# Kernel optimization log

Measured on AMD Instinct MI355X. Metric: run time of the kernel, lower is better.

Reference implementation:

```python
import jax, jax.numpy as jnp
import numpy as np

EMB_DIM = 1024
N_HEADS = 16
N_KV_GROUPS = 4
GROUP_SIZE = N_HEADS // N_KV_GROUPS
HEAD_DIM = EMB_DIM // N_HEADS
KV_DIM = N_KV_GROUPS * HEAD_DIM
B, S = 2, 2048


def setup_inputs() -> dict:
    key = jax.random.key(0)
    ks = jax.random.split(key, 6)
    sc = 0.02
    return {
        "x": jax.random.normal(ks[0], (B, S, EMB_DIM), dtype=jnp.float32),
        "Wq": jax.random.normal(ks[1], (EMB_DIM, EMB_DIM), dtype=jnp.float32) * sc,
        "Wk": jax.random.normal(ks[2], (EMB_DIM, KV_DIM), dtype=jnp.float32) * sc,
        "Wv": jax.random.normal(ks[3], (EMB_DIM, KV_DIM), dtype=jnp.float32) * sc,
        "Wo": jax.random.normal(ks[4], (EMB_DIM, EMB_DIM), dtype=jnp.float32) * sc,
        "bo": jax.random.normal(ks[5], (EMB_DIM,), dtype=jnp.float32) * sc,
    }


def reference(x, Wq, Wk, Wv, Wo, bo):
    b, s, _ = x.shape
    # projections
    q = (x @ Wq).reshape(b, s, N_HEADS, HEAD_DIM).transpose(0, 2, 1, 3)      # [b,H,s,d]
    k = (x @ Wk).reshape(b, s, N_KV_GROUPS, HEAD_DIM).transpose(0, 2, 1, 3)  # [b,G,s,d]
    v = (x @ Wv).reshape(b, s, N_KV_GROUPS, HEAD_DIM).transpose(0, 2, 1, 3)
    # repeat_interleave KV heads to match query heads
    k = jnp.repeat(k, GROUP_SIZE, axis=1)  # [b,H,s,d]
    v = jnp.repeat(v, GROUP_SIZE, axis=1)
    scores = jnp.einsum("bhqd,bhkd->bhqk", q, k)  # [b,H,s,s]
    causal = jnp.triu(jnp.ones((s, s), dtype=bool), k=1)
    scores = jnp.where(causal, -jnp.inf, scores)
    attn = jax.nn.softmax(scores / np.sqrt(HEAD_DIM).astype(np.float32), axis=-1)
    ctx = jnp.einsum("bhqk,bhkd->bhqd", attn, v)  # [b,H,s,d]
    ctx = ctx.transpose(0, 2, 1, 3).reshape(b, s, EMB_DIM)
    return ctx @ Wo + bo
```

## Files before the change

### kernel.cpp

```cpp
#include <hip/hip_runtime.h>
#include <hip/hip_bf16.h>


typedef __attribute__((ext_vector_type(8))) short          bf16x8;
typedef __attribute__((ext_vector_type(4))) float          f32x4;
typedef __attribute__((ext_vector_type(4))) unsigned short u16x4;
typedef __attribute__((ext_vector_type(8))) unsigned short u16x8;

#define DEV __device__ __forceinline__

static constexpr int BB   = 2;
static constexpr int SS   = 2048;
static constexpr int EMB  = 1024;
static constexpr int QKVD = 1536;
static constexpr float SC2 = 0.18033688011112042f;
static constexpr float M2C = 16.0f;

DEV unsigned short f2b(float f) {
  union { float f; unsigned u; } v; v.f = f;
  unsigned r = (v.u + 0x7FFFu + ((v.u >> 16) & 1u)) >> 16;
  return (unsigned short)r;
}

DEV unsigned packbf2(float a, float b) {
  __hip_bfloat162 h = __float22bfloat162_rn(make_float2(a, b));
  union { __hip_bfloat162 h; unsigned u; } c; c.h = h; return c.u;
}

DEV void gl_lds16(const void* g, void* l) {
  __builtin_amdgcn_global_load_lds((__attribute__((address_space(1))) void*)g,
                                   (__attribute__((address_space(3))) void*)l,
                                   16, 0, 0);
}

__global__ __launch_bounds__(256) void prep_kernel(const float* __restrict__ x,
                                                   unsigned short* __restrict__ xb,
                                                   const float* __restrict__ Wq,
                                                   const float* __restrict__ Wk,
                                                   const float* __restrict__ Wv,
                                                   const float* __restrict__ Wo,
                                                   unsigned short* __restrict__ Wqkv_t,
                                                   unsigned short* __restrict__ Wo_t) {
  __shared__ unsigned short tile[64][72];
  const int blk = blockIdx.x;
  const int tid = threadIdx.x;
  if (blk < 2048) {
    size_t i = ((size_t)blk * 256 + tid) * 8;
    f32x4 f0 = *(const f32x4*)(x + i);
    f32x4 f1 = *(const f32x4*)(x + i + 4);
    u16x8 o;
    o[0] = f2b(f0[0]); o[1] = f2b(f0[1]); o[2] = f2b(f0[2]); o[3] = f2b(f0[3]);
    o[4] = f2b(f1[0]); o[5] = f2b(f1[1]); o[6] = f2b(f1[2]); o[7] = f2b(f1[3]);
    *(u16x8*)(xb + i) = o;
    return;
  }
  int idx = blk - 2048;
  const float* W; unsigned short* Dst; int N, kb, nb;
  if (idx < 256)      { W = Wq; Dst = Wqkv_t;                       N = 1024; kb = idx >> 4; nb = idx & 15; }
  else if (idx < 320) { int j = idx - 256; W = Wk; Dst = Wqkv_t + (size_t)1024 * 1024; N = 256; kb = j >> 2; nb = j & 3; }
  else if (idx < 384) { int j = idx - 320; W = Wv; Dst = Wqkv_t + (size_t)1280 * 1024; N = 256; kb = j >> 2; nb = j & 3; }
  else                { int j = idx - 384; W = Wo; Dst = Wo_t;      N = 1024; kb = j >> 4; nb = j & 15; }
  const int kb64 = kb * 64, nb64 = nb * 64;
#pragma unroll
  for (int p = 0; p < 16; ++p) {
    int i = tid + 256 * p;
    int k = i >> 6, n = i & 63;
    tile[k][n] = f2b(W[(size_t)(kb64 + k) * N + nb64 + n]);
  }
  __syncthreads();
#pragma unroll
  for (int p = 0; p < 16; ++p) {
    int i = tid + 256 * p;
    int n = i >> 6, k = i & 63;
    Dst[(size_t)(nb64 + n) * 1024 + kb64 + k] = tile[k][n];
  }
}

__global__ __launch_bounds__(256) void transpose_v(const unsigned short* __restrict__ QKV,
                                                   unsigned short* __restrict__ Vt) {
  __shared__ unsigned short t[64][72];
  const int s0 = blockIdx.x * 64;
  const int bg = blockIdx.y;
  const int b = bg >> 2, g = bg & 3;
  const int tid = threadIdx.x;
#pragma unroll
  for (int p = 0; p < 2; ++p) {
    int i = tid + 256 * p;
    int si = i >> 3, d0 = (i & 7) * 8;
    bf16x8 v = *(const bf16x8*)(QKV + ((size_t)(b * SS + s0 + si)) * QKVD + 1280 + g * 64 + d0);
#pragma unroll
    for (int j = 0; j < 8; ++j) t[si][d0 + j] = (unsigned short)v[j];
  }
  __syncthreads();
#pragma unroll
  for (int p = 0; p < 2; ++p) {
    int i = tid + 256 * p;
    int d = i >> 3, sv = (i & 7) * 8;
    bf16x8 vv;
#pragma unroll
    for (int j = 0; j < 8; ++j) vv[j] = (short)t[sv + j][d];
    *(bf16x8*)(Vt + ((size_t)(bg * 64 + d)) * SS + s0 + sv) = vv;
  }
}

template <bool BF16_OUT, bool BIAS>
__global__ __launch_bounds__(256) void gemm64(const unsigned short* __restrict__ A,
                                              const unsigned short* __restrict__ Bt,
                                              void* __restrict__ Cv,
                                              const float* __restrict__ bias,
                                              int Nc, int Kd) {
  const int tid = threadIdx.x;
  const int w = tid >> 6, lane = tid & 63;
  const int l15 = lane & 15, l4 = lane >> 4;
  const int wr = w >> 1, wc = w & 1;
  const size_t rb = (size_t)blockIdx.x * 64;
  const size_t cb = (size_t)blockIdx.y * 128;

  __shared__ alignas(16) unsigned short sA[2][64 * 64];
  __shared__ alignas(16) unsigned short sB[2][128 * 64];

  f32x4 acc[2][4] = {};

  const int srow = tid >> 3;
  const int scg = ((tid & 7) ^ (srow & 7)) * 8;
  const unsigned short* Ap = A + (rb + srow) * (size_t)Kd + scg;
  const unsigned short* Bp = Bt + (cb + srow) * (size_t)Kd + scg;

  auto STAGE = [&](int kt, int bsel) {
    const size_t off = (size_t)kt * 64;
    gl_lds16(Ap + off,                    (char*)sA + bsel * 8192 + tid * 16);
    gl_lds16(Ap + off + (size_t)32 * Kd,  (char*)sA + bsel * 8192 + 4096 + tid * 16);
#pragma unroll
    for (int i = 0; i < 4; ++i)
      gl_lds16(Bp + off + (size_t)(32 * i) * Kd,
               (char*)sB + bsel * 16384 + i * 4096 + tid * 16);
  };

  const int KT = Kd >> 6;
  STAGE(0, 0);
  STAGE(1, 1);
  asm volatile("s_waitcnt vmcnt(6)" ::: "memory");
  __builtin_amdgcn_s_barrier();

  const int xk = l15 & 7;
  for (int kt = 0; kt < KT; ++kt) {
    const int cur = kt & 1;
#pragma unroll
    for (int kk = 0; kk < 2; ++kk) {
      const int ck = ((kk * 4 + l4) ^ xk) * 8;
      bf16x8 af[2], bfr[4];
#pragma unroll
      for (int m = 0; m < 2; ++m)
        af[m] = *(const bf16x8*)&sA[cur][(wr * 32 + m * 16 + l15) * 64 + ck];
#pragma unroll
      for (int n = 0; n < 4; ++n)
        bfr[n] = *(const bf16x8*)&sB[cur][(wc * 64 + n * 16 + l15) * 64 + ck];
#pragma unroll
      for (int m = 0; m < 2; ++m)
#pragma unroll
        for (int n = 0; n < 4; ++n)
          acc[m][n] = __builtin_amdgcn_mfma_f32_16x16x32_bf16(af[m], bfr[n], acc[m][n], 0, 0, 0);
    }

    __builtin_amdgcn_s_barrier();
    if (kt + 2 < KT) {
      STAGE(kt + 2, cur);
      asm volatile("s_waitcnt vmcnt(6)" ::: "memory");
    } else {
      asm volatile("s_waitcnt vmcnt(0)" ::: "memory");
    }
    __builtin_amdgcn_s_barrier();
  }

#pragma unroll
  for (int m = 0; m < 2; ++m)
#pragma unroll
    for (int n = 0; n < 4; ++n) {
      float bv = 0.f;
      if constexpr (BIAS) bv = bias[cb + wc * 64 + n * 16 + l15];
#pragma unroll
      for (int r = 0; r < 4; ++r) {
        size_t row = rb + wr * 32 + m * 16 + 4 * l4 + r;
        size_t col = cb + wc * 64 + n * 16 + l15;
        if constexpr (BF16_OUT)
          ((unsigned short*)Cv)[row * Nc + col] = f2b(acc[m][n][r]);
        else
          ((float*)Cv)[row * Nc + col] = acc[m][n][r] + bv;
      }
    }
}

struct QS {
  bf16x8 qf0, qf1;
  f32x4 o[4];
  f32x4 l4;
  int qg;
};

DEV void qs_init(QS& s, const unsigned short* __restrict__ QKV,
                 int b, int h, int row0, int l15, int l4) {
  s.qg = row0 + l15;
  const unsigned short* qp =
      QKV + ((size_t)(b * SS + row0 + l15)) * QKVD + h * 64 + 8 * l4;
  s.qf0 = *(const bf16x8*)qp;
  s.qf1 = *(const bf16x8*)(qp + 32);
#pragma unroll
  for (int t = 0; t < 4; ++t) s.o[t] = f32x4{0.f, 0.f, 0.f, 0.f};
  s.l4 = f32x4{0.f, 0.f, 0.f, 0.f};
}

DEV void qs_tile(QS& st, const unsigned short* __restrict__ sKc,
                 const unsigned short* __restrict__ sVc,
                 int kv0, bool masked, const bf16x8& ones,
                 int l15, int l4, int xsw, int s0, int s1, bool hi) {
  f32x4 p[4];
#pragma unroll
  for (int c = 0; c < 4; ++c) {
    const unsigned short* krow = &sKc[(c * 16 + l15) * 64];
    bf16x8 kf0 = *(const bf16x8*)&krow[(l4 ^ xsw) * 8];
    bf16x8 kf1 = *(const bf16x8*)&krow[((4 | l4) ^ xsw) * 8];
    f32x4 z = {0.f, 0.f, 0.f, 0.f};
    z = __builtin_amdgcn_mfma_f32_16x16x32_bf16(kf0, st.qf0, z, 0, 0, 0);
    z = __builtin_amdgcn_mfma_f32_16x16x32_bf16(kf1, st.qf1, z, 0, 0, 0);
    p[c] = z;
  }

  if (masked) {
#pragma unroll
    for (int c = 0; c < 4; ++c)
#pragma unroll
      for (int r = 0; r < 4; ++r) {
        int kv = kv0 + c * 16 + 4 * l4 + r;
        if (kv > st.qg) p[c][r] = -3e38f;
      }
  }

  unsigned w0[4], w1[4];
#pragma unroll
  for (int c = 0; c < 4; ++c) {
    w0[c] = packbf2(exp2f(fmaf(p[c][0], SC2, -M2C)),
                    exp2f(fmaf(p[c][1], SC2, -M2C)));
    w1[c] = packbf2(exp2f(fmaf(p[c][2], SC2, -M2C)),
                    exp2f(fmaf(p[c][3], SC2, -M2C)));
  }

#pragma unroll
  for (int ks = 0; ks < 2; ++ks) {
    unsigned a00 = __shfl(w0[2 * ks], s0), a01 = __shfl(w0[2 * ks + 1], s0);
    unsigned a10 = __shfl(w1[2 * ks], s0), a11 = __shfl(w1[2 * ks + 1], s0);
    unsigned b00 = __shfl(w0[2 * ks], s1), b01 = __shfl(w0[2 * ks + 1], s1);
    unsigned b10 = __shfl(w1[2 * ks], s1), b11 = __shfl(w1[2 * ks + 1], s1);
    union { bf16x8 v; unsigned u[4]; } pf;
    pf.u[0] = hi ? a01 : a00;
    pf.u[1] = hi ? a11 : a10;
    pf.u[2] = hi ? b01 : b00;
    pf.u[3] = hi ? b11 : b10;
#pragma unroll
    for (int t = 0; t < 4; ++t) {
      const unsigned short* vrow = &sVc[(t * 16 + l15) * 64];
      bf16x8 vf = *(const bf16x8*)&vrow[((4 * ks + l4) ^ xsw) * 8];
      st.o[t] = __builtin_amdgcn_mfma_f32_16x16x32_bf16(pf.v, vf, st.o[t], 0, 0, 0);
    }
    st.l4 = __builtin_amdgcn_mfma_f32_16x16x32_bf16(pf.v, ones, st.l4, 0, 0, 0);
  }
}

DEV void qs_write(const QS& st, unsigned short* __restrict__ Ctx,
                  int b, int h, int row0, int l15, int l4) {
  f32x4 inv;
#pragma unroll
  for (int r = 0; r < 4; ++r) inv[r] = 1.f / st.l4[r];
#pragma unroll
  for (int t = 0; t < 4; ++t)
#pragma unroll
    for (int r = 0; r < 4; ++r) {
      Ctx[((size_t)(b * SS + row0 + 4 * l4 + r)) * 1024 + h * 64 + t * 16 + l15] =
          f2b(st.o[t][r] * inv[r]);
    }
}

__global__ __launch_bounds__(256, 4) void attn_kernel(const unsigned short* __restrict__ QKV,
                                                      const unsigned short* __restrict__ Vt,
                                                      unsigned short* __restrict__ Ctx) {
  const int f = blockIdx.x;
  const int xcd = f & 7;
  const int b = xcd >> 2, g = xcd & 3;
  const int h = g * 4 + ((f >> 3) & 3);
  const int qt = 31 - (f >> 5);
  const int nkv = qt + 1;

  const int tid = threadIdx.x;
  const int w = tid >> 6, lane = tid & 63;
  const int l15 = lane & 15, l4 = lane >> 4;
  const int row0 = qt * 64 + w * 16;

  __shared__ alignas(16) unsigned short sK[2][64 * 64];
  __shared__ alignas(16) unsigned short sV[2][64 * 64];

  QS A;
  qs_init(A, QKV, b, h, row0, l15, l4);

  const short oneb = (short)0x3F80;
  bf16x8 ones = {oneb, oneb, oneb, oneb, oneb, oneb, oneb, oneb};

  const int srow = tid >> 3;
  const int scg = ((tid & 7) ^ (srow & 7)) * 8;
  const unsigned short* kbase =
      QKV + ((size_t)(b * SS + srow)) * QKVD + 1024 + g * 64 + scg;
  const unsigned short* vbase =
      Vt + ((size_t)(((b << 2) | g) * 64 + srow)) * SS + scg;

  auto STAGE = [&](int t, int bsel) {
    const size_t kvoff = (size_t)(64 * t);
#pragma unroll
    for (int i = 0; i < 2; ++i)
      gl_lds16(kbase + (kvoff + 32 * i) * QKVD,
               (char*)sK + bsel * 8192 + i * 4096 + tid * 16);
#pragma unroll
    for (int i = 0; i < 2; ++i)
      gl_lds16(vbase + (size_t)(32 * i) * SS + kvoff,
               (char*)sV + bsel * 8192 + i * 4096 + tid * 16);
  };

  const int xsw = (l15 & 7);
  const int s0 = l15 | (((2 * l4) & 3) << 4);
  const int s1 = l15 | (((2 * l4 + 1) & 3) << 4);
  const bool hi = (l4 >= 2);

  STAGE(0, 0);
  STAGE(1, 1);
  asm volatile("s_waitcnt vmcnt(4)" ::: "memory");
  __builtin_amdgcn_s_barrier();

  for (int kt = 0; kt < nkv; ++kt) {
    const int cur = kt & 1;
    qs_tile(A, &sK[cur][0], &sV[cur][0], kt * 64, kt == nkv - 1, ones,
            l15, l4, xsw, s0, s1, hi);

    __builtin_amdgcn_s_barrier();
    if (kt + 2 < nkv) {
      STAGE(kt + 2, cur);
      asm volatile("s_waitcnt vmcnt(4)" ::: "memory");
    } else {
      asm volatile("s_waitcnt vmcnt(0)" ::: "memory");
    }
    __builtin_amdgcn_s_barrier();
  }

  qs_write(A, Ctx, b, h, row0, l15, l4);
}

extern "C" void kernel_launch(void* const* d_in, const int* in_sizes, int n_in,
                              void* d_out, int out_size, void* d_ws, size_t ws_size,
                              hipStream_t stream) {
  (void)in_sizes; (void)n_in; (void)out_size; (void)ws_size;
  const float* x  = (const float*)d_in[0];
  const float* Wq = (const float*)d_in[1];
  const float* Wk = (const float*)d_in[2];
  const float* Wv = (const float*)d_in[3];
  const float* Wo = (const float*)d_in[4];
  const float* bo = (const float*)d_in[5];
  float* out = (float*)d_out;

  char* ws = (char*)d_ws;
  unsigned short* x_bf   = (unsigned short*)(ws);
  unsigned short* Ctx    = (unsigned short*)(ws);
  unsigned short* QKVb   = (unsigned short*)(ws + (size_t)( 8u << 20));
  unsigned short* Wqkv_t = (unsigned short*)(ws + (size_t)(20u << 20));
  unsigned short* Wo_t   = (unsigned short*)(ws + (size_t)(23u << 20));
  unsigned short* Vtb    = (unsigned short*)(ws + (size_t)(25u << 20));

  prep_kernel<<<dim3(2688), 256, 0, stream>>>(x, x_bf, Wq, Wk, Wv, Wo, Wqkv_t, Wo_t);

  gemm64<true, false><<<dim3(64, 12), 256, 0, stream>>>(
      x_bf, Wqkv_t, QKVb, nullptr, QKVD, EMB);

  transpose_v<<<dim3(32, 8), 256, 0, stream>>>(QKVb, Vtb);

  attn_kernel<<<dim3(1024), 256, 0, stream>>>(QKVb, Vtb, Ctx);

  gemm64<false, true><<<dim3(64, 8), 256, 0, stream>>>(
      Ctx, Wo_t, out, bo, EMB, EMB);
}
```

Measured before the change: 96.24 us.

## Fuse V transpose into QKV GEMM epilogue and reorder attention tile schedule

```diff
diff --git a/kernel.cpp b/kernel.cpp
--- a/kernel.cpp
+++ b/kernel.cpp
@@ -76,38 +76,12 @@
   }
 }
 
-__global__ __launch_bounds__(256) void transpose_v(const unsigned short* __restrict__ QKV,
-                                                   unsigned short* __restrict__ Vt) {
-  __shared__ unsigned short t[64][72];
-  const int s0 = blockIdx.x * 64;
-  const int bg = blockIdx.y;
-  const int b = bg >> 2, g = bg & 3;
-  const int tid = threadIdx.x;
-#pragma unroll
-  for (int p = 0; p < 2; ++p) {
-    int i = tid + 256 * p;
-    int si = i >> 3, d0 = (i & 7) * 8;
-    bf16x8 v = *(const bf16x8*)(QKV + ((size_t)(b * SS + s0 + si)) * QKVD + 1280 + g * 64 + d0);
-#pragma unroll
-    for (int j = 0; j < 8; ++j) t[si][d0 + j] = (unsigned short)v[j];
-  }
-  __syncthreads();
-#pragma unroll
-  for (int p = 0; p < 2; ++p) {
-    int i = tid + 256 * p;
-    int d = i >> 3, sv = (i & 7) * 8;
-    bf16x8 vv;
-#pragma unroll
-    for (int j = 0; j < 8; ++j) vv[j] = (short)t[sv + j][d];
-    *(bf16x8*)(Vt + ((size_t)(bg * 64 + d)) * SS + s0 + sv) = vv;
-  }
-}
-
-template <bool BF16_OUT, bool BIAS>
+template <bool BF16_OUT, bool BIAS, bool VT>
 __global__ __launch_bounds__(256) void gemm64(const unsigned short* __restrict__ A,
                                               const unsigned short* __restrict__ Bt,
                                               void* __restrict__ Cv,
                                               const float* __restrict__ bias,
+                                              unsigned short* __restrict__ vt,
                                               int Nc, int Kd) {
   const int tid = threadIdx.x;
   const int w = tid >> 6, lane = tid & 63;
@@ -170,6 +144,27 @@
       asm volatile("s_waitcnt vmcnt(0)" ::: "memory");
     }
     __builtin_amdgcn_s_barrier();
+  }
+
+  if constexpr (VT) {
+    if (blockIdx.y >= 10) {
+      const int b = (int)(rb >> 11);
+      const int s0 = (int)(rb & 2047);
+      const int g = 2 * ((int)blockIdx.y - 10) + wc;
+#pragma unroll
+      for (int m = 0; m < 2; ++m)
+#pragma unroll
+        for (int n = 0; n < 4; ++n) {
+          const size_t vtrow = (size_t)((b * 4 + g) * 64 + n * 16 + l15);
+          u16x4 v;
+          v[0] = f2b(acc[m][n][0]);
+          v[1] = f2b(acc[m][n][1]);
+          v[2] = f2b(acc[m][n][2]);
+          v[3] = f2b(acc[m][n][3]);
+          *(u16x4*)(vt + vtrow * SS + s0 + wr * 32 + m * 16 + 4 * l4) = v;
+        }
+      return;
+    }
   }
 
 #pragma unroll
@@ -286,7 +281,9 @@
   const int xcd = f & 7;
   const int b = xcd >> 2, g = xcd & 3;
   const int h = g * 4 + ((f >> 3) & 3);
-  const int qt = 31 - (f >> 5);
+  const int s5 = f >> 5;
+  const int g5 = s5 & 7, pp = s5 >> 3;
+  const int qt = (pp == 0) ? 31 - g5 : (pp == 1) ? 16 + g5 : (pp == 2) ? 15 - g5 : g5;
   const int nkv = qt + 1;
 
   const int tid = threadIdx.x;
@@ -372,13 +369,11 @@
 
   prep_kernel<<<dim3(2688), 256, 0, stream>>>(x, x_bf, Wq, Wk, Wv, Wo, Wqkv_t, Wo_t);
 
-  gemm64<true, false><<<dim3(64, 12), 256, 0, stream>>>(
-      x_bf, Wqkv_t, QKVb, nullptr, QKVD, EMB);
-
-  transpose_v<<<dim3(32, 8), 256, 0, stream>>>(QKVb, Vtb);
+  gemm64<true, false, true><<<dim3(64, 12), 256, 0, stream>>>(
+      x_bf, Wqkv_t, QKVb, nullptr, Vtb, QKVD, EMB);
 
   attn_kernel<<<dim3(1024), 256, 0, stream>>>(QKVb, Vtb, Ctx);
 
-  gemm64<false, true><<<dim3(64, 8), 256, 0, stream>>>(
-      Ctx, Wo_t, out, bo, EMB, EMB);
-}
+  gemm64<false, true, false><<<dim3(64, 8), 256, 0, stream>>>(
+      Ctx, Wo_t, out, bo, nullptr, EMB, EMB);
+}
```

Result: faster. 91.84 us (-4.6%).
